# Performance work log

Hardware: AMD Instinct MI355X
Metric: run time of the kernel (lower is better)

## Reference

```python
import jax, jax.numpy as jnp
import numpy as np

NEG_SLOPE = 0.01  # torch F.leaky_relu default

def _lrelu(x):
    return jax.nn.leaky_relu(x, NEG_SLOPE)

def setup_inputs() -> dict:
    key = jax.random.key(0)
    ks = jax.random.split(key, 24)
    B, N, E = 512, 20000, 640000
    n_enc_1, n_enc_2, n_z = 512, 256, 64
    n_dec_2, n_dec_1, hidden = 256, 512, 256
    p = lambda k, shp, fan: jax.random.normal(k, shp, jnp.float32) * (1.0 / np.sqrt(fan))
    return {
        "data": jax.random.normal(ks[0], (B, N), jnp.float32),
        "noise": jax.random.normal(ks[1], (B, N), jnp.float32),
        "edge_index": jax.random.randint(ks[2], (2, E), 0, N, jnp.int32),
        "w_gcn": jax.random.normal(ks[3], (), jnp.float32),
        "b_gcn": jax.random.normal(ks[4], (), jnp.float32) * 0.1,
        "enc1_w": p(ks[5], (N, n_enc_1), N), "enc1_b": p(ks[6], (n_enc_1,), N),
        "enc2_w": p(ks[7], (n_enc_1, n_enc_2), n_enc_1), "enc2_b": p(ks[8], (n_enc_2,), n_enc_1),
        "enc3_w": p(ks[9], (n_enc_2, n_z), n_enc_2), "enc3_b": p(ks[10], (n_z,), n_enc_2),
        "dec1_w": p(ks[11], (n_z, n_dec_2), n_z), "dec1_b": p(ks[12], (n_dec_2,), n_z),
        "dec2_w": p(ks[13], (n_dec_2, n_dec_1), n_dec_2), "dec2_b": p(ks[14], (n_dec_1,), n_dec_2),
        "dec3_w": p(ks[15], (n_dec_1, N), n_dec_1), "dec3_b": p(ks[16], (N,), n_dec_1),
        "disc1_w": p(ks[17], (n_z, hidden), n_z), "disc1_b": p(ks[18], (hidden,), n_z),
        "disc2_w": p(ks[19], (hidden, hidden), hidden), "disc2_b": p(ks[20], (hidden,), hidden),
        "disc3_w": p(ks[21], (hidden, 1), hidden), "disc3_b": p(ks[22], (1,), hidden),
    }

def _gcn_batched(x, edge_index, w_gcn, b_gcn):
    # x: [B, N] -> GCNConv(1,1, improved=True) applied per row, vectorized.
    B, N = x.shape
    src, dst = edge_index[0], edge_index[1]
    loop = jnp.arange(N, dtype=src.dtype)
    src_a = jnp.concatenate([src, loop])
    dst_a = jnp.concatenate([dst, loop])
    # improved=True: self-loop edge weight 2.0
    ew = jnp.concatenate([jnp.ones(src.shape[0], x.dtype), jnp.full((N,), 2.0, x.dtype)])
    deg = jax.ops.segment_sum(ew, dst_a, num_segments=N)
    dinv = jnp.where(deg > 0, jax.lax.rsqrt(deg), 0.0)
    norm = dinv[src_a] * ew * dinv[dst_a]  # [E+N]
    xl = x * w_gcn                         # lin (1x1 weight, no bias)
    msgs = xl[:, src_a] * norm[None, :]    # [B, E+N]
    agg = jnp.zeros_like(x).at[:, dst_a].add(msgs)
    return agg + b_gcn

def reference(data, noise, edge_index, w_gcn, b_gcn,
              enc1_w, enc1_b, enc2_w, enc2_b, enc3_w, enc3_b,
              dec1_w, dec1_b, dec2_w, dec2_b, dec3_w, dec3_b,
              disc1_w, disc1_b, disc2_w, disc2_b, disc3_w, disc3_b):
    x = data + noise * 0.1
    gcn_out = _lrelu(_gcn_batched(x, edge_index, w_gcn, b_gcn))  # [B, N]
    h1 = _lrelu(gcn_out @ enc1_w + enc1_b)
    h2 = _lrelu(h1 @ enc2_w + enc2_b)
    z = _lrelu(h2 @ enc3_w + enc3_b)
    d1 = _lrelu(z @ dec1_w + dec1_b)
    d2 = _lrelu(d1 @ dec2_w + dec2_b)
    dec_h3 = _lrelu(d2 @ dec3_w + dec3_b)
    g1 = _lrelu(z @ disc1_w + disc1_b)
    g2 = _lrelu(g1 @ disc2_w + disc2_b)
    d = jax.nn.sigmoid(g2 @ disc3_w + disc3_b)
    return (dec_h3, z, d)
```

## Files before the change

kernel.cpp:

```cpp
#include <hip/hip_runtime.h>
#include <hip/hip_bf16.h>


#define LRELU(v) ((v) > 0.f ? (v) : 0.01f * (v))

static constexpr int Bb = 512;
static constexpr int Nn = 20000;
static constexpr int Ee = 640000;
static constexpr int KBn = 2500;
static constexpr int NPD = 20096;

typedef __attribute__((ext_vector_type(8))) short short8;
typedef __attribute__((ext_vector_type(4))) float f32x4;

__device__ __forceinline__ ushort f2bf(float f) {
  uint u = __builtin_bit_cast(uint, f);
  u = u + 0x7FFFu + ((u >> 16) & 1u);
  return (ushort)(u >> 16);
}
__device__ __forceinline__ float bfLo(uint u) {
  return __builtin_bit_cast(float, u << 16);
}
__device__ __forceinline__ float bfHi(uint u) {
  return __builtin_bit_cast(float, u & 0xffff0000u);
}

__global__ void transpose_xs_k(const float* __restrict__ a, const float* __restrict__ nz,
                               const float* __restrict__ dinv, ushort* __restrict__ xs) {
  __shared__ ushort tile[64][65];
  int c0 = blockIdx.x * 64;
  int p = blockIdx.y;
  int chunk = p >> 1;
  int sub = (p & 1) * 64;
  int rbase = p * 64;
  for (int i = threadIdx.x; i < 64 * 64; i += 256) {
    int rr = i >> 6, cc = i & 63;
    int r = rbase + rr, c = c0 + cc;
    ushort v = 0;
    if (c < Nn) {
      size_t idx = (size_t)r * Nn + c;
      v = f2bf(dinv[c] * (a[idx] + 0.1f * nz[idx]));
    }
    tile[rr][cc] = v;
  }
  __syncthreads();
  for (int i = threadIdx.x; i < 64 * 64; i += 256) {
    int cc = i >> 6, rr = i & 63;
    int c = c0 + cc;
    if (c < Nn) xs[(size_t)chunk * Nn * 128 + (size_t)c * 128 + sub + rr] = tile[rr][cc];
  }
}

__global__ void hist_check_k(const int* __restrict__ src, const int* __restrict__ dst, int E,
                             int* __restrict__ cnt, int* __restrict__ flag) {
  int i = blockIdx.x * 256 + threadIdx.x;
  if (i < E) {
    int s = src[i], d = dst[i];
    if ((unsigned)s >= (unsigned)Nn || (unsigned)d >= (unsigned)Nn) {
      atomicExch(flag, 1);
    } else {
      atomicAdd(&cnt[d], 1);
    }
  }
}

__global__ void offs_k(const int* __restrict__ cnt, int* __restrict__ offs,
                       int* __restrict__ cursor, float* __restrict__ dinv,
                       int* __restrict__ bump) {
  int i = blockIdx.x * 256 + threadIdx.x;
  int l = threadIdx.x & 63;
  int v = (i < Nn) ? cnt[i] : 0;
  int x = v;
#pragma unroll
  for (int d = 1; d < 64; d <<= 1) {
    int t = __shfl_up(x, d);
    if (l >= d) x += t;
  }
  int total = __shfl(x, 63);
  int base = 0;
  if (l == 0) base = atomicAdd(bump, total);
  base = __shfl(base, 0);
  int excl = base + x - v;
  if (i < Nn) {
    offs[i] = excl;
    cursor[i] = excl;
    dinv[i] = rsqrtf(2.0f + (float)v);
  }
}

__global__ void scatter_k(const int* __restrict__ src, const int* __restrict__ dst, int E,
                          int* __restrict__ cursor, uint* __restrict__ eOff) {
  int i = blockIdx.x * 256 + threadIdx.x;
  if (i < E) {
    int s = src[i], d = dst[i];
    if ((unsigned)s >= (unsigned)Nn || (unsigned)d >= (unsigned)Nn) return;
    int p = atomicAdd(&cursor[d], 1);
    eOff[p] = (uint)s * 256u;
  }
}

__global__ __launch_bounds__(256) void spmm_fm_k(
    const ushort* __restrict__ xs, const uint* __restrict__ eOff, const int* __restrict__ offs,
    const int* __restrict__ cnt, const float* __restrict__ dinv, const float* __restrict__ wg,
    const float* __restrict__ bg, ushort* __restrict__ gfm) {
  __shared__ uint sIdx[4][64];
  __shared__ ushort sOut[128][8];
  int bid = blockIdx.x;
  int chunk = bid & 3;
  int grp = bid >> 2;
  int wv = threadIdx.x >> 6, l = threadIdx.x & 63;
  const char* base = (const char*)(xs + (size_t)chunk * Nn * 128) + l * 4;
  float wgv = wg[0], bb = bg[0];

#pragma unroll
  for (int sub = 0; sub < 2; ++sub) {
    int n = grp * 8 + wv * 2 + sub;
    int o = offs[n], c = cnt[n];
    const uint* ep = eOff + o;
    uint su = *(const uint*)(base + (size_t)n * 256);
    float a00 = 2.0f * bfLo(su), a01 = 2.0f * bfHi(su);
    float a10 = 0.f, a11 = 0.f;

    for (int bi = 0; bi < c; bi += 64) {
      int rem = c - bi;
      if (rem > 64) rem = 64;
      sIdx[wv][l] = (l < rem) ? ep[bi + l] : 0u;
      int i = 0;
      for (; i + 8 <= rem; i += 8) {
        uint u[8];
#pragma unroll
        for (int j = 0; j < 8; ++j) u[j] = *(const uint*)(base + sIdx[wv][i + j]);
#pragma unroll
        for (int j = 0; j < 8; j += 2) {
          a00 += bfLo(u[j]);
          a01 += bfHi(u[j]);
          a10 += bfLo(u[j + 1]);
          a11 += bfHi(u[j + 1]);
        }
      }
      for (; i < rem; ++i) {
        uint u = *(const uint*)(base + sIdx[wv][i]);
        a00 += bfLo(u);
        a01 += bfHi(u);
      }
    }

    float wdn = wgv * dinv[n];
    float v0 = wdn * (a00 + a10) + bb;
    float v1 = wdn * (a01 + a11) + bb;
    v0 = LRELU(v0);
    v1 = LRELU(v1);
    int j = wv * 2 + sub;
    sOut[2 * l][j] = f2bf(v0);
    sOut[2 * l + 1][j] = f2bf(v1);
  }
  __syncthreads();
  int row = threadIdx.x >> 1, half = threadIdx.x & 1;
  uint2 v = *(const uint2*)&sOut[row][half * 4];
  int m = chunk * 128 + row;
  *(uint2*)&gfm[((size_t)grp * 512 + m) * 8 + half * 4] = v;
}

__global__ void conv_we_k(const float* __restrict__ W, ushort* __restrict__ wef) {
  int n = blockIdx.x * 256 + threadIdx.x;
  int kb = blockIdx.y;
  ushort v[8];
#pragma unroll
  for (int j = 0; j < 8; ++j) v[j] = f2bf(W[(size_t)(8 * kb + j) * 512 + n]);
  uint4 pk;
  pk.x = (uint)v[0] | ((uint)v[1] << 16);
  pk.y = (uint)v[2] | ((uint)v[3] << 16);
  pk.z = (uint)v[4] | ((uint)v[5] << 16);
  pk.w = (uint)v[6] | ((uint)v[7] << 16);
  *(uint4*)&wef[((size_t)kb * 512 + n) * 8] = pk;
}

__global__ __launch_bounds__(256) void fmg_enc1_k(const ushort* __restrict__ gfm,
                                                  const ushort* __restrict__ wef,
                                                  float* __restrict__ C) {
  int n0 = blockIdx.x * 128, m0 = blockIdx.y * 128;
  int l = threadIdx.x & 63, w = threadIdx.x >> 6;
  int wr = w >> 1, wc = w & 1;
  int lrow = l & 15, lkg = l >> 4;
  f32x4 acc[4][4] = {};
  int ksBeg = blockIdx.z * 25, ksEnd = ksBeg + 25;

  for (int ks = ksBeg; ks < ksEnd; ++ks) {
    int kb = ks * 4 + lkg;
    short8 a[4], b[4];
#pragma unroll
    for (int mi = 0; mi < 4; ++mi) {
      int m = m0 + wr * 64 + mi * 16 + lrow;
      a[mi] = *(const short8*)&gfm[((size_t)kb * 512 + m) * 8];
    }
#pragma unroll
    for (int nj = 0; nj < 4; ++nj) {
      int n = n0 + wc * 64 + nj * 16 + lrow;
      b[nj] = *(const short8*)&wef[((size_t)kb * 512 + n) * 8];
    }
#pragma unroll
    for (int mi = 0; mi < 4; ++mi)
#pragma unroll
      for (int nj = 0; nj < 4; ++nj)
        acc[mi][nj] = __builtin_amdgcn_mfma_f32_16x16x32_bf16(a[mi], b[nj], acc[mi][nj], 0, 0, 0);
  }

#pragma unroll
  for (int mi = 0; mi < 4; ++mi)
#pragma unroll
    for (int nj = 0; nj < 4; ++nj)
#pragma unroll
      for (int r = 0; r < 4; ++r) {
        int row = m0 + wr * 64 + mi * 16 + lkg * 4 + r;
        int col = n0 + wc * 64 + nj * 16 + lrow;
        atomicAdd(&C[(size_t)row * 512 + col], acc[mi][nj][r]);
      }
}

__global__ void conv_wf_k(const float* __restrict__ W, ushort* __restrict__ wf) {
  int n = blockIdx.x * 256 + threadIdx.x;
  int kb = blockIdx.y;
  if (n >= NPD) return;
  ushort v[8];
#pragma unroll
  for (int j = 0; j < 8; ++j)
    v[j] = (n < Nn) ? f2bf(W[(size_t)(8 * kb + j) * Nn + n]) : (ushort)0;
  uint4 pk;
  pk.x = (uint)v[0] | ((uint)v[1] << 16);
  pk.y = (uint)v[2] | ((uint)v[3] << 16);
  pk.z = (uint)v[4] | ((uint)v[5] << 16);
  pk.w = (uint)v[6] | ((uint)v[7] << 16);
  *(uint4*)&wf[((size_t)kb * NPD + n) * 8] = pk;
}

__global__ __launch_bounds__(256) void fmg_dec3_k(const ushort* __restrict__ d2f,
                                                  const ushort* __restrict__ wf,
                                                  const float* __restrict__ bias,
                                                  float* __restrict__ C) {
  int n0 = blockIdx.x * 128, m0 = blockIdx.y * 128;
  int l = threadIdx.x & 63, w = threadIdx.x >> 6;
  int wr = w >> 1, wc = w & 1;
  int lrow = l & 15, lkg = l >> 4;
  f32x4 acc[4][4] = {};

#pragma unroll 4
  for (int ks = 0; ks < 16; ++ks) {
    int kb = ks * 4 + lkg;
    short8 a[4], b[4];
#pragma unroll
    for (int mi = 0; mi < 4; ++mi) {
      int m = m0 + wr * 64 + mi * 16 + lrow;
      a[mi] = *(const short8*)&d2f[((size_t)kb * 512 + m) * 8];
    }
#pragma unroll
    for (int nj = 0; nj < 4; ++nj) {
      int n = n0 + wc * 64 + nj * 16 + lrow;
      b[nj] = *(const short8*)&wf[((size_t)kb * NPD + n) * 8];
    }
#pragma unroll
    for (int mi = 0; mi < 4; ++mi)
#pragma unroll
      for (int nj = 0; nj < 4; ++nj)
        acc[mi][nj] = __builtin_amdgcn_mfma_f32_16x16x32_bf16(a[mi], b[nj], acc[mi][nj], 0, 0, 0);
  }

#pragma unroll
  for (int mi = 0; mi < 4; ++mi)
#pragma unroll
    for (int nj = 0; nj < 4; ++nj)
#pragma unroll
      for (int r = 0; r < 4; ++r) {
        int row = m0 + wr * 64 + mi * 16 + lkg * 4 + r;
        int col = n0 + wc * 64 + nj * 16 + lrow;
        if (col < Nn) {
          float v = acc[mi][nj][r] + bias[col];
          C[(size_t)row * Nn + col] = LRELU(v);
        }
      }
}

__global__ __launch_bounds__(256) void tail2_k(
    const float* __restrict__ h1, const float* __restrict__ c1, const float* __restrict__ W2,
    const float* __restrict__ c2, const float* __restrict__ W3, const float* __restrict__ c3,
    const float* __restrict__ Wd1, const float* __restrict__ cd1, const float* __restrict__ Wd2,
    const float* __restrict__ cd2, const float* __restrict__ Wg1, const float* __restrict__ cg1,
    const float* __restrict__ Wg2, const float* __restrict__ cg2, const float* __restrict__ Wg3,
    const float* __restrict__ cg3, float* __restrict__ out_z, float* __restrict__ out_d,
    ushort* __restrict__ d2f) {
  __shared__ float s_h1[512];
  __shared__ float s_h2[256];
  __shared__ float s_z[64];
  __shared__ float s_d1[256];
  __shared__ float s_g1[256];
  __shared__ float s_g2[256];
  __shared__ float s_part[4][256];
  __shared__ float s_red[4];
  int rl = blockIdx.x;
  int t = threadIdx.x;
  int w = t >> 6, l = t & 63;

  {
    float r0 = h1[(size_t)rl * 512 + t] + c1[t];
    float r1 = h1[(size_t)rl * 512 + t + 256] + c1[t + 256];
    s_h1[t] = LRELU(r0);
    s_h1[t + 256] = LRELU(r1);
  }
  __syncthreads();

  {
    int c4 = l * 4;
    float a0 = 0.f, a1 = 0.f, a2 = 0.f, a3 = 0.f;
#pragma unroll 8
    for (int k = w * 128; k < w * 128 + 128; ++k) {
      float4 wv = *(const float4*)&W2[(size_t)k * 256 + c4];
      float x = s_h1[k];
      a0 += x * wv.x; a1 += x * wv.y; a2 += x * wv.z; a3 += x * wv.w;
    }
    float4 pv = {a0, a1, a2, a3};
    *(float4*)&s_part[w][c4] = pv;
  }
  __syncthreads();
  s_h2[t] = LRELU(s_part[0][t] + s_part[1][t] + s_part[2][t] + s_part[3][t] + c2[t]);
  __syncthreads();

  {
    int c = t >> 2, p = t & 3;
    float a = 0.f;
#pragma unroll 8
    for (int k = p * 64; k < p * 64 + 64; ++k) a += s_h2[k] * W3[(size_t)k * 64 + c];
    s_part[p][c] = a;
  }
  __syncthreads();
  if (t < 64) {
    float v = s_part[0][t] + s_part[1][t] + s_part[2][t] + s_part[3][t] + c3[t];
    v = LRELU(v);
    s_z[t] = v;
    out_z[(size_t)rl * 64 + t] = v;
  }
  __syncthreads();

  {
    float a = 0.f;
#pragma unroll
    for (int k = 0; k < 64; ++k) a += s_z[k] * Wd1[(size_t)k * 256 + t];
    s_d1[t] = LRELU(a + cd1[t]);
  }
  {
    float a = 0.f;
#pragma unroll
    for (int k = 0; k < 64; ++k) a += s_z[k] * Wg1[(size_t)k * 256 + t];
    s_g1[t] = LRELU(a + cg1[t]);
  }
  __syncthreads();

  {
    int g = t & 127, p = t >> 7;
    int c4 = g * 4;
    float a0 = 0.f, a1 = 0.f, a2 = 0.f, a3 = 0.f;
#pragma unroll 8
    for (int k = p * 128; k < p * 128 + 128; ++k) {
      float4 wv = *(const float4*)&Wd2[(size_t)k * 512 + c4];
      float x = s_d1[k];
      a0 += x * wv.x; a1 += x * wv.y; a2 += x * wv.z; a3 += x * wv.w;
    }
    float* sp = &s_part[0][0];
    float4 pv = {a0, a1, a2, a3};
    *(float4*)&sp[p * 512 + c4] = pv;
  }
  __syncthreads();
  {
    const float* sp = &s_part[0][0];
#pragma unroll
    for (int cc = 0; cc < 2; ++cc) {
      int c = t + cc * 256;
      float v = sp[c] + sp[512 + c] + cd2[c];
      v = LRELU(v);
      d2f[((size_t)(c >> 3) * 512 + rl) * 8 + (c & 7)] = f2bf(v);
    }
  }
  __syncthreads();

  {
    int c4 = l * 4;
    float a0 = 0.f, a1 = 0.f, a2 = 0.f, a3 = 0.f;
#pragma unroll 8
    for (int k = w * 64; k < w * 64 + 64; ++k) {
      float4 wv = *(const float4*)&Wg2[(size_t)k * 256 + c4];
      float x = s_g1[k];
      a0 += x * wv.x; a1 += x * wv.y; a2 += x * wv.z; a3 += x * wv.w;
    }
    float4 pv = {a0, a1, a2, a3};
    *(float4*)&s_part[w][c4] = pv;
  }
  __syncthreads();
  s_g2[t] = LRELU(s_part[0][t] + s_part[1][t] + s_part[2][t] + s_part[3][t] + cg2[t]);
  __syncthreads();

  {
    float p = s_g2[t] * Wg3[t];
#pragma unroll
    for (int o = 32; o > 0; o >>= 1) p += __shfl_down(p, o);
    if ((t & 63) == 0) s_red[t >> 6] = p;
    __syncthreads();
    if (t == 0) {
      float s = s_red[0] + s_red[1] + s_red[2] + s_red[3] + cg3[0];
      out_d[rl] = 1.f / (1.f + __expf(-s));
    }
  }
}

__global__ void sentinel_k(float* out, float val) { out[0] = val; }
__global__ void flag_sentinel_k(float* out, const int* flag) {
  if (*flag != 0) out[0] = 70000.0f;
}

extern "C" void kernel_launch(void* const* d_in, const int* in_sizes, int n_in,
                              void* d_out, int out_size, void* d_ws, size_t ws_size,
                              hipStream_t stream) {
  const float* data = (const float*)d_in[0];
  const float* noise = (const float*)d_in[1];
  const int* edge = (const int*)d_in[2];
  const int* esrc_in = edge;
  const int* edst_in = edge + Ee;
  const float* w_gcn = (const float*)d_in[3];
  const float* b_gcn = (const float*)d_in[4];
  const float* enc1_w = (const float*)d_in[5];
  const float* enc1_b = (const float*)d_in[6];
  const float* enc2_w = (const float*)d_in[7];
  const float* enc2_b = (const float*)d_in[8];
  const float* enc3_w = (const float*)d_in[9];
  const float* enc3_b = (const float*)d_in[10];
  const float* dec1_w = (const float*)d_in[11];
  const float* dec1_b = (const float*)d_in[12];
  const float* dec2_w = (const float*)d_in[13];
  const float* dec2_b = (const float*)d_in[14];
  const float* dec3_w = (const float*)d_in[15];
  const float* dec3_b = (const float*)d_in[16];
  const float* disc1_w = (const float*)d_in[17];
  const float* disc1_b = (const float*)d_in[18];
  const float* disc2_w = (const float*)d_in[19];
  const float* disc2_b = (const float*)d_in[20];
  const float* disc3_w = (const float*)d_in[21];
  const float* disc3_b = (const float*)d_in[22];

  char* w = (char*)d_ws;
  size_t o = 0;
  auto alloc = [&](size_t bytes) {
    size_t r = o;
    o = (o + bytes + 15) & ~(size_t)15;
    return r;
  };
  size_t r1 = alloc((size_t)64 * NPD * 8 * 2);
  ushort* xs = (ushort*)(w + r1);
  ushort* wef = (ushort*)(w + r1);
  ushort* wf = (ushort*)(w + r1);
  ushort* gfm = (ushort*)(w + alloc((size_t)KBn * 512 * 8 * 2));
  float* h1 = (float*)(w + alloc(512 * 512 * 4));
  ushort* d2f = (ushort*)(w + alloc((size_t)64 * 512 * 8 * 2));
  float* dinv = (float*)(w + alloc(Nn * 4));
  int* cnt = (int*)(w + alloc(Nn * 4));
  int* offs = (int*)(w + alloc(Nn * 4));
  int* cursor = (int*)(w + alloc(Nn * 4));
  uint* eOff = (uint*)(w + alloc(Ee * 4));
  int* flag = (int*)(w + alloc(16));

  float* outp = (float*)d_out;
  float* out_dec = outp;
  float* out_z = outp + (size_t)Bb * Nn;
  float* out_d = out_z + (size_t)Bb * 64;

  static const int expect_sizes[23] = {
      10240000, 10240000, 1280000, 1, 1,
      10240000, 512, 131072, 256, 16384, 64,
      16384, 256, 131072, 512, 10240000, 20000,
      16384, 256, 65536, 256, 256, 1};
  float host_sentinel = 0.f;
  if (n_in != 23) host_sentinel = 50000.f;
  else if (out_size != 10273280) host_sentinel = 80000.f;
  else if (ws_size < 46100000u) host_sentinel = 60000.f;
  else {
    for (int i = 0; i < 23; ++i)
      if (in_sizes[i] != expect_sizes[i]) { host_sentinel = 100000.f + 1000.f * i; break; }
  }

  hipMemsetAsync(cnt, 0, Nn * sizeof(int), stream);
  hipMemsetAsync(flag, 0, 2 * sizeof(int), stream);
  hist_check_k<<<(Ee + 255) / 256, 256, 0, stream>>>(esrc_in, edst_in, Ee, cnt, flag);
  offs_k<<<(Nn + 255) / 256, 256, 0, stream>>>(cnt, offs, cursor, dinv, flag + 1);
  scatter_k<<<(Ee + 255) / 256, 256, 0, stream>>>(esrc_in, edst_in, Ee, cursor, eOff);

  {
    dim3 g((Nn + 63) / 64, 8);
    transpose_xs_k<<<g, 256, 0, stream>>>(data, noise, dinv, xs);
  }
  spmm_fm_k<<<(Nn / 8) * 4, 256, 0, stream>>>(xs, eOff, offs, cnt, dinv, w_gcn, b_gcn, gfm);
  {
    dim3 g(2, KBn);
    conv_we_k<<<g, 256, 0, stream>>>(enc1_w, wef);
  }
  hipMemsetAsync(h1, 0, 512 * 512 * 4, stream);
  {
    dim3 g(512 / 128, 512 / 128, 25);
    fmg_enc1_k<<<g, 256, 0, stream>>>(gfm, wef, h1);
  }
  tail2_k<<<Bb, 256, 0, stream>>>(h1, enc1_b, enc2_w, enc2_b, enc3_w, enc3_b, dec1_w, dec1_b,
                                  dec2_w, dec2_b, disc1_w, disc1_b, disc2_w, disc2_b, disc3_w,
                                  disc3_b, out_z, out_d, d2f);
  {
    dim3 g((NPD + 255) / 256, 64);
    conv_wf_k<<<g, 256, 0, stream>>>(dec3_w, wf);
  }
  {
    dim3 g(NPD / 128, 512 / 128);
    fmg_dec3_k<<<g, 256, 0, stream>>>(d2f, wf, dec3_b, out_dec);
  }

  flag_sentinel_k<<<1, 1, 0, stream>>>(out_dec, flag);
  if (host_sentinel != 0.f) sentinel_k<<<1, 1, 0, stream>>>(out_dec, host_sentinel);
}
```

Baseline: 288.9 us.

## Process two rows per tail block and deepen SpMM gather unroll

The tail MLP kernel now handles two batch rows per block, so every weight load from global memory feeds two rows' accumulators and the number of blocks is halved. The SpMM gather loop is unrolled to 16 loads with a 4-wide remainder loop, raising memory-level parallelism on the indirect loads. The h1 memset moves to the start of the stream. The cost is more registers and fewer blocks (256) for the tail kernel, which may reduce latency hiding.

```diff
diff --git a/kernel.cpp b/kernel.cpp
--- a/kernel.cpp
+++ b/kernel.cpp
@@ -126,17 +126,31 @@
       if (rem > 64) rem = 64;
       sIdx[wv][l] = (l < rem) ? ep[bi + l] : 0u;
       int i = 0;
-      for (; i + 8 <= rem; i += 8) {
-        uint u[8];
-#pragma unroll
-        for (int j = 0; j < 8; ++j) u[j] = *(const uint*)(base + sIdx[wv][i + j]);
-#pragma unroll
-        for (int j = 0; j < 8; j += 2) {
+      for (; i + 16 <= rem; i += 16) {
+        uint u[16];
+#pragma unroll
+        for (int j = 0; j < 16; ++j) u[j] = *(const uint*)(base + sIdx[wv][i + j]);
+#pragma unroll
+        for (int j = 0; j < 16; j += 2) {
           a00 += bfLo(u[j]);
           a01 += bfHi(u[j]);
           a10 += bfLo(u[j + 1]);
           a11 += bfHi(u[j + 1]);
         }
+      }
+      for (; i + 4 <= rem; i += 4) {
+        uint u0 = *(const uint*)(base + sIdx[wv][i]);
+        uint u1 = *(const uint*)(base + sIdx[wv][i + 1]);
+        uint u2 = *(const uint*)(base + sIdx[wv][i + 2]);
+        uint u3 = *(const uint*)(base + sIdx[wv][i + 3]);
+        a00 += bfLo(u0);
+        a01 += bfHi(u0);
+        a10 += bfLo(u1);
+        a11 += bfHi(u1);
+        a00 += bfLo(u2);
+        a01 += bfHi(u2);
+        a10 += bfLo(u3);
+        a11 += bfHi(u3);
       }
       for (; i < rem; ++i) {
         uint u = *(const uint*)(base + sIdx[wv][i]);
@@ -279,7 +293,7 @@
       }
 }
 
-__global__ __launch_bounds__(256) void tail2_k(
+__global__ __launch_bounds__(256) void tail4_k(
     const float* __restrict__ h1, const float* __restrict__ c1, const float* __restrict__ W2,
     const float* __restrict__ c2, const float* __restrict__ W3, const float* __restrict__ c3,
     const float* __restrict__ Wd1, const float* __restrict__ cd1, const float* __restrict__ Wd2,
@@ -287,124 +301,169 @@
     const float* __restrict__ Wg2, const float* __restrict__ cg2, const float* __restrict__ Wg3,
     const float* __restrict__ cg3, float* __restrict__ out_z, float* __restrict__ out_d,
     ushort* __restrict__ d2f) {
-  __shared__ float s_h1[512];
-  __shared__ float s_h2[256];
-  __shared__ float s_z[64];
-  __shared__ float s_d1[256];
-  __shared__ float s_g1[256];
-  __shared__ float s_g2[256];
-  __shared__ float s_part[4][256];
-  __shared__ float s_red[4];
-  int rl = blockIdx.x;
+  __shared__ float s_h1[2][512];
+  __shared__ float s_h2[2][256];
+  __shared__ float s_z[2][64];
+  __shared__ float s_d1[2][256];
+  __shared__ float s_g1[2][256];
+  __shared__ float s_g2[2][256];
+  __shared__ float s_part[2048];
+  __shared__ float s_red[4][2];
+  int rl0 = blockIdx.x * 2;
   int t = threadIdx.x;
   int w = t >> 6, l = t & 63;
 
-  {
-    float r0 = h1[(size_t)rl * 512 + t] + c1[t];
-    float r1 = h1[(size_t)rl * 512 + t + 256] + c1[t + 256];
-    s_h1[t] = LRELU(r0);
-    s_h1[t + 256] = LRELU(r1);
+#pragma unroll
+  for (int r = 0; r < 2; ++r) {
+    float v0 = h1[(size_t)(rl0 + r) * 512 + t] + c1[t];
+    float v1 = h1[(size_t)(rl0 + r) * 512 + t + 256] + c1[t + 256];
+    s_h1[r][t] = LRELU(v0);
+    s_h1[r][t + 256] = LRELU(v1);
   }
   __syncthreads();
 
   {
     int c4 = l * 4;
-    float a0 = 0.f, a1 = 0.f, a2 = 0.f, a3 = 0.f;
-#pragma unroll 8
+    float a00 = 0.f, a01 = 0.f, a02 = 0.f, a03 = 0.f;
+    float a10 = 0.f, a11 = 0.f, a12 = 0.f, a13 = 0.f;
+#pragma unroll 4
     for (int k = w * 128; k < w * 128 + 128; ++k) {
       float4 wv = *(const float4*)&W2[(size_t)k * 256 + c4];
-      float x = s_h1[k];
-      a0 += x * wv.x; a1 += x * wv.y; a2 += x * wv.z; a3 += x * wv.w;
-    }
-    float4 pv = {a0, a1, a2, a3};
-    *(float4*)&s_part[w][c4] = pv;
-  }
-  __syncthreads();
-  s_h2[t] = LRELU(s_part[0][t] + s_part[1][t] + s_part[2][t] + s_part[3][t] + c2[t]);
+      float x0 = s_h1[0][k], x1 = s_h1[1][k];
+      a00 += x0 * wv.x; a01 += x0 * wv.y; a02 += x0 * wv.z; a03 += x0 * wv.w;
+      a10 += x1 * wv.x; a11 += x1 * wv.y; a12 += x1 * wv.z; a13 += x1 * wv.w;
+    }
+    float4 p0 = {a00, a01, a02, a03};
+    float4 p1 = {a10, a11, a12, a13};
+    *(float4*)&s_part[(w * 2 + 0) * 256 + c4] = p0;
+    *(float4*)&s_part[(w * 2 + 1) * 256 + c4] = p1;
+  }
+  __syncthreads();
+#pragma unroll
+  for (int r = 0; r < 2; ++r)
+    s_h2[r][t] = LRELU(s_part[r * 256 + t] + s_part[(2 + r) * 256 + t] +
+                       s_part[(4 + r) * 256 + t] + s_part[(6 + r) * 256 + t] + c2[t]);
   __syncthreads();
 
   {
     int c = t >> 2, p = t & 3;
-    float a = 0.f;
+    float a0 = 0.f, a1 = 0.f;
 #pragma unroll 8
-    for (int k = p * 64; k < p * 64 + 64; ++k) a += s_h2[k] * W3[(size_t)k * 64 + c];
-    s_part[p][c] = a;
-  }
-  __syncthreads();
-  if (t < 64) {
-    float v = s_part[0][t] + s_part[1][t] + s_part[2][t] + s_part[3][t] + c3[t];
+    for (int k = p * 64; k < p * 64 + 64; ++k) {
+      float wv = W3[(size_t)k * 64 + c];
+      a0 += s_h2[0][k] * wv;
+      a1 += s_h2[1][k] * wv;
+    }
+    s_part[(p * 2 + 0) * 64 + c] = a0;
+    s_part[(p * 2 + 1) * 64 + c] = a1;
+  }
+  __syncthreads();
+  if (t < 128) {
+    int r = t >> 6, c = t & 63;
+    float v = s_part[(0 * 2 + r) * 64 + c] + s_part[(1 * 2 + r) * 64 + c] +
+              s_part[(2 * 2 + r) * 64 + c] + s_part[(3 * 2 + r) * 64 + c] + c3[c];
     v = LRELU(v);
-    s_z[t] = v;
-    out_z[(size_t)rl * 64 + t] = v;
-  }
-  __syncthreads();
-
-  {
-    float a = 0.f;
-#pragma unroll
-    for (int k = 0; k < 64; ++k) a += s_z[k] * Wd1[(size_t)k * 256 + t];
-    s_d1[t] = LRELU(a + cd1[t]);
-  }
-  {
-    float a = 0.f;
-#pragma unroll
-    for (int k = 0; k < 64; ++k) a += s_z[k] * Wg1[(size_t)k * 256 + t];
-    s_g1[t] = LRELU(a + cg1[t]);
+    s_z[r][c] = v;
+    out_z[(size_t)(rl0 + r) * 64 + c] = v;
+  }
+  __syncthreads();
+
+  {
+    float a0 = 0.f, a1 = 0.f;
+#pragma unroll
+    for (int k = 0; k < 64; ++k) {
+      float wv = Wd1[(size_t)k * 256 + t];
+      a0 += s_z[0][k] * wv;
+      a1 += s_z[1][k] * wv;
+    }
+    s_d1[0][t] = LRELU(a0 + cd1[t]);
+    s_d1[1][t] = LRELU(a1 + cd1[t]);
+  }
+  {
+    float a0 = 0.f, a1 = 0.f;
+#pragma unroll
+    for (int k = 0; k < 64; ++k) {
+      float wv = Wg1[(size_t)k * 256 + t];
+      a0 += s_z[0][k] * wv;
+      a1 += s_z[1][k] * wv;
+    }
+    s_g1[0][t] = LRELU(a0 + cg1[t]);
+    s_g1[1][t] = LRELU(a1 + cg1[t]);
   }
   __syncthreads();
 
   {
     int g = t & 127, p = t >> 7;
     int c4 = g * 4;
-    float a0 = 0.f, a1 = 0.f, a2 = 0.f, a3 = 0.f;
-#pragma unroll 8
+    float a00 = 0.f, a01 = 0.f, a02 = 0.f, a03 = 0.f;
+    float a10 = 0.f, a11 = 0.f, a12 = 0.f, a13 = 0.f;
+#pragma unroll 4
     for (int k = p * 128; k < p * 128 + 128; ++k) {
       float4 wv = *(const float4*)&Wd2[(size_t)k * 512 + c4];
-      float x = s_d1[k];
-      a0 += x * wv.x; a1 += x * wv.y; a2 += x * wv.z; a3 += x * wv.w;
-    }
-    float* sp = &s_part[0][0];
-    float4 pv = {a0, a1, a2, a3};
-    *(float4*)&sp[p * 512 + c4] = pv;
-  }
-  __syncthreads();
-  {
-    const float* sp = &s_part[0][0];
+      float x0 = s_d1[0][k], x1 = s_d1[1][k];
+      a00 += x0 * wv.x; a01 += x0 * wv.y; a02 += x0 * wv.z; a03 += x0 * wv.w;
+      a10 += x1 * wv.x; a11 += x1 * wv.y; a12 += x1 * wv.z; a13 += x1 * wv.w;
+    }
+    float4 p0 = {a00, a01, a02, a03};
+    float4 p1 = {a10, a11, a12, a13};
+    *(float4*)&s_part[(p * 2 + 0) * 512 + c4] = p0;
+    *(float4*)&s_part[(p * 2 + 1) * 512 + c4] = p1;
+  }
+  __syncthreads();
+  {
 #pragma unroll
     for (int cc = 0; cc < 2; ++cc) {
       int c = t + cc * 256;
-      float v = sp[c] + sp[512 + c] + cd2[c];
-      v = LRELU(v);
-      d2f[((size_t)(c >> 3) * 512 + rl) * 8 + (c & 7)] = f2bf(v);
+#pragma unroll
+      for (int r = 0; r < 2; ++r) {
+        float v = s_part[(0 * 2 + r) * 512 + c] + s_part[(1 * 2 + r) * 512 + c] + cd2[c];
+        v = LRELU(v);
+        d2f[((size_t)(c >> 3) * 512 + (rl0 + r)) * 8 + (c & 7)] = f2bf(v);
+      }
     }
   }
   __syncthreads();
 
   {
     int c4 = l * 4;
-    float a0 = 0.f, a1 = 0.f, a2 = 0.f, a3 = 0.f;
-#pragma unroll 8
+    float a00 = 0.f, a01 = 0.f, a02 = 0.f, a03 = 0.f;
+    float a10 = 0.f, a11 = 0.f, a12 = 0.f, a13 = 0.f;
+#pragma unroll 4
     for (int k = w * 64; k < w * 64 + 64; ++k) {
       float4 wv = *(const float4*)&Wg2[(size_t)k * 256 + c4];
-      float x = s_g1[k];
-      a0 += x * wv.x; a1 += x * wv.y; a2 += x * wv.z; a3 += x * wv.w;
-    }
-    float4 pv = {a0, a1, a2, a3};
-    *(float4*)&s_part[w][c4] = pv;
-  }
-  __syncthreads();
-  s_g2[t] = LRELU(s_part[0][t] + s_part[1][t] + s_part[2][t] + s_part[3][t] + cg2[t]);
-  __syncthreads();
-
-  {
-    float p = s_g2[t] * Wg3[t];
-#pragma unroll
-    for (int o = 32; o > 0; o >>= 1) p += __shfl_down(p, o);
-    if ((t & 63) == 0) s_red[t >> 6] = p;
+      float x0 = s_g1[0][k], x1 = s_g1[1][k];
+      a00 += x0 * wv.x; a01 += x0 * wv.y; a02 += x0 * wv.z; a03 += x0 * wv.w;
+      a10 += x1 * wv.x; a11 += x1 * wv.y; a12 += x1 * wv.z; a13 += x1 * wv.w;
+    }
+    float4 p0 = {a00, a01, a02, a03};
+    float4 p1 = {a10, a11, a12, a13};
+    *(float4*)&s_part[(w * 2 + 0) * 256 + c4] = p0;
+    *(float4*)&s_part[(w * 2 + 1) * 256 + c4] = p1;
+  }
+  __syncthreads();
+#pragma unroll
+  for (int r = 0; r < 2; ++r)
+    s_g2[r][t] = LRELU(s_part[r * 256 + t] + s_part[(2 + r) * 256 + t] +
+                       s_part[(4 + r) * 256 + t] + s_part[(6 + r) * 256 + t] + cg2[t]);
+  __syncthreads();
+
+  {
+    float wv = Wg3[t];
+    float p0 = s_g2[0][t] * wv;
+    float p1 = s_g2[1][t] * wv;
+#pragma unroll
+    for (int o = 32; o > 0; o >>= 1) {
+      p0 += __shfl_down(p0, o);
+      p1 += __shfl_down(p1, o);
+    }
+    if (l == 0) {
+      s_red[w][0] = p0;
+      s_red[w][1] = p1;
+    }
     __syncthreads();
-    if (t == 0) {
-      float s = s_red[0] + s_red[1] + s_red[2] + s_red[3] + cg3[0];
-      out_d[rl] = 1.f / (1.f + __expf(-s));
+    if (t < 2) {
+      float s = s_red[0][t] + s_red[1][t] + s_red[2][t] + s_red[3][t] + cg3[0];
+      out_d[rl0 + t] = 1.f / (1.f + __expf(-s));
     }
   }
 }
@@ -485,6 +544,7 @@
 
   hipMemsetAsync(cnt, 0, Nn * sizeof(int), stream);
   hipMemsetAsync(flag, 0, 2 * sizeof(int), stream);
+  hipMemsetAsync(h1, 0, 512 * 512 * 4, stream);
   hist_check_k<<<(Ee + 255) / 256, 256, 0, stream>>>(esrc_in, edst_in, Ee, cnt, flag);
   offs_k<<<(Nn + 255) / 256, 256, 0, stream>>>(cnt, offs, cursor, dinv, flag + 1);
   scatter_k<<<(Ee + 255) / 256, 256, 0, stream>>>(esrc_in, edst_in, Ee, cursor, eOff);
@@ -498,14 +558,13 @@
     dim3 g(2, KBn);
     conv_we_k<<<g, 256, 0, stream>>>(enc1_w, wef);
   }
-  hipMemsetAsync(h1, 0, 512 * 512 * 4, stream);
   {
     dim3 g(512 / 128, 512 / 128, 25);
     fmg_enc1_k<<<g, 256, 0, stream>>>(gfm, wef, h1);
   }
-  tail2_k<<<Bb, 256, 0, stream>>>(h1, enc1_b, enc2_w, enc2_b, enc3_w, enc3_b, dec1_w, dec1_b,
-                                  dec2_w, dec2_b, disc1_w, disc1_b, disc2_w, disc2_b, disc3_w,
-                                  disc3_b, out_z, out_d, d2f);
+  tail4_k<<<Bb / 2, 256, 0, stream>>>(h1, enc1_b, enc2_w, enc2_b, enc3_w, enc3_b, dec1_w,
+                                      dec1_b, dec2_w, dec2_b, disc1_w, disc1_b, disc2_w,
+                                      disc2_b, disc3_w, disc3_b, out_z, out_d, d2f);
   {
     dim3 g((NPD + 255) / 256, 64);
     conv_wf_k<<<g, 256, 0, stream>>>(dec3_w, wf);
```

New measurement: 280.4 us. 2.9% less time.
